# Kernel optimization log

Measured on AMD Instinct MI355X. Metric: run time of the kernel, lower is better.

The kernel has to match this reference:

```python
import jax, jax.numpy as jnp
import numpy as np

H = 4096   # hidden_size
V = 4      # vocab_size (Dyck-2)
OUT = 4    # output_size
MS = 104   # memory_size (stack depth)
MD = 3     # memory_dim (stack element width)


def setup_inputs() -> dict:
    key = jax.random.key(0)
    ks = jax.random.split(key, 17)
    s = 1.0 / np.sqrt(H)
    f32 = jnp.float32
    return {
        "inp": jax.random.randint(ks[0], (1,), 0, H),
        "hidden0": jax.random.normal(ks[1], (1, 1, H), f32),
        "stack": jax.random.normal(ks[2], (MS, MD), f32),
        "emb": (jax.random.normal(ks[3], (H, V), f32) * s),      # nn.Embedding(H, V)
        "w_ih": (jax.random.normal(ks[4], (3 * H, V), f32) * s),  # GRU input weights
        "w_hh": (jax.random.normal(ks[5], (3 * H, H), f32) * s),  # GRU hidden weights
        "b_ih": (jax.random.normal(ks[6], (3 * H,), f32) * s),
        "b_hh": (jax.random.normal(ks[7], (3 * H,), f32) * s),
        "w_y": (jax.random.normal(ks[8], (OUT, H), f32) * s),
        "b_y": (jax.random.normal(ks[9], (OUT,), f32) * s),
        "w_n": (jax.random.normal(ks[10], (MD, H), f32) * s),
        "b_n": (jax.random.normal(ks[11], (MD,), f32) * s),
        "w_a": (jax.random.normal(ks[12], (2, H), f32) * s),
        "b_a": (jax.random.normal(ks[13], (2,), f32) * s),
        "w_sh": (jax.random.normal(ks[14], (H, MD), f32) * s),
        "b_sh": (jax.random.normal(ks[15], (H,), f32) * s),
    }


def reference(inp, hidden0, stack, emb, w_ih, w_hh, b_ih, b_hh,
              w_y, b_y, w_n, b_n, w_a, b_a, w_sh, b_sh):
    # embedded = embedding(inp).view(1,1,-1) -> work with flat (V,)
    x = emb[inp[0]]                                   # (V,)
    # hidden_bar = W_sh(stack[0]) + hidden0
    h_bar = (w_sh @ stack[0] + b_sh) + hidden0[0, 0]  # (H,)
    # one GRU step (PyTorch gate order: r, z, n)
    gi = w_ih @ x + b_ih                              # (3H,)
    gh = w_hh @ h_bar + b_hh                          # (3H,)
    i_r, i_z, i_n = jnp.split(gi, 3)
    h_r, h_z, h_n = jnp.split(gh, 3)
    r = jax.nn.sigmoid(i_r + h_r)
    z = jax.nn.sigmoid(i_z + h_z)
    n = jnp.tanh(i_n + r * h_n)
    h = (1.0 - z) * n + z * h_bar                     # (H,) = ht = hidden
    # heads
    output = jax.nn.sigmoid(w_y @ h + b_y).reshape(1, OUT)
    action = jax.nn.softmax(w_a @ h + b_a)            # (2,) push/pop weights
    new_elt = jax.nn.sigmoid(w_n @ h + b_n).reshape(1, MD)
    # differentiable stack update
    push_side = jnp.concatenate([new_elt, stack[:-1]], axis=0)          # (MS, MD)
    pop_side = jnp.concatenate([stack[1:], jnp.zeros((1, MD), stack.dtype)], axis=0)
    new_stack = action[0] * push_side + action[1] * pop_side
    hidden = h.reshape(1, 1, H)
    return output, hidden, new_stack
```

## Files before the change

### kernel.cpp

```cpp
#include <hip/hip_runtime.h>
#include <hip/hip_bf16.h>

#define H  4096
#define V  4
#define OUT_N 4
#define MS 104
#define MD 3

__device__ __forceinline__ float b2f(unsigned short u) {
    return __uint_as_float(((unsigned int)u) << 16);
}
__device__ __forceinline__ float ldf(const void* p, size_t i, bool is_f32) {
    return is_f32 ? ((const float*)p)[i] : b2f(((const unsigned short*)p)[i]);
}
__device__ __forceinline__ void stf(void* p, size_t i, bool is_f32, float v) {
    if (is_f32) ((float*)p)[i] = v;
    else        ((__hip_bfloat16*)p)[i] = __float2bfloat16(v);
}

__global__ void detect_kernel(const unsigned short* __restrict__ w_hh_raw,
                              int* __restrict__ flag) {
    const int t = threadIdx.x;
    int bad = 0;
    for (int i = t; i < 1024; i += 64) {
        const float v = b2f(w_hh_raw[i]);
        if (!(fabsf(v) < 1.0e6f)) bad = 1;
    }
    const unsigned long long m = __ballot(bad);
    if (t == 0) flag[0] = (m != 0ull) ? 1 : 0;
}

__global__ __launch_bounds__(256) void hbar_kernel(
    const void* __restrict__ w_sh, const void* __restrict__ b_sh,
    const void* __restrict__ hidden0, const void* __restrict__ stack,
    const int* __restrict__ flag, float* __restrict__ h_bar) {
    const bool f32 = flag[0] != 0;
    const float s0 = ldf(stack, 0, f32);
    const float s1 = ldf(stack, 1, f32);
    const float s2 = ldf(stack, 2, f32);
    const int j = blockIdx.x * 256 + threadIdx.x;
    if (j < H) {
        h_bar[j] = ldf(w_sh, (size_t)j * 3 + 0, f32) * s0
                 + ldf(w_sh, (size_t)j * 3 + 1, f32) * s1
                 + ldf(w_sh, (size_t)j * 3 + 2, f32) * s2
                 + ldf(b_sh, j, f32) + ldf(hidden0, j, f32);
    }
}

__global__ __launch_bounds__(256) void gru_kernel(
    const int*  __restrict__ inp,  const void* __restrict__ emb,
    const void* __restrict__ w_ih, const void* __restrict__ w_hh,
    const void* __restrict__ b_ih, const void* __restrict__ b_hh,
    const int*  __restrict__ flag, const float* __restrict__ h_bar,
    float* __restrict__ h_f32, void* __restrict__ out) {
    const bool f32 = flag[0] != 0;
    const int k = blockIdx.x, t = threadIdx.x;
    const size_t r0 = (size_t)k * H;
    const size_t r1 = (size_t)(k + H) * H;
    const size_t r2 = (size_t)(k + 2 * H) * H;

    float ar = 0.f, az = 0.f, an = 0.f;
    #pragma unroll 4
    for (int i = t; i < H; i += 256) {
        const float hb = h_bar[i];
        ar += ldf(w_hh, r0 + i, f32) * hb;
        az += ldf(w_hh, r1 + i, f32) * hb;
        an += ldf(w_hh, r2 + i, f32) * hb;
    }

    #pragma unroll
    for (int off = 32; off > 0; off >>= 1) {
        ar += __shfl_down(ar, off);
        az += __shfl_down(az, off);
        an += __shfl_down(an, off);
    }
    __shared__ float red[4][3];
    const int wave = t >> 6, lane = t & 63;
    if (lane == 0) { red[wave][0] = ar; red[wave][1] = az; red[wave][2] = an; }
    __syncthreads();

    if (t == 0) {
        const float sr = red[0][0] + red[1][0] + red[2][0] + red[3][0];
        const float sz = red[0][1] + red[1][1] + red[2][1] + red[3][1];
        const float sn = red[0][2] + red[1][2] + red[2][2] + red[3][2];

        const int idx = inp[0];
        float x[V];
        #pragma unroll
        for (int c = 0; c < V; ++c) x[c] = ldf(emb, (size_t)idx * V + c, f32);

        float gi[3];
        #pragma unroll
        for (int g = 0; g < 3; ++g) {
            float acc = ldf(b_ih, (size_t)(k + g * H), f32);
            #pragma unroll
            for (int c = 0; c < V; ++c)
                acc += ldf(w_ih, (size_t)(k + g * H) * V + c, f32) * x[c];
            gi[g] = acc;
        }
        const float ghr = sr + ldf(b_hh, (size_t)k,         f32);
        const float ghz = sz + ldf(b_hh, (size_t)(k + H),   f32);
        const float ghn = sn + ldf(b_hh, (size_t)(k + 2*H), f32);

        const float r = 1.f / (1.f + expf(-(gi[0] + ghr)));
        const float z = 1.f / (1.f + expf(-(gi[1] + ghz)));
        const float n = tanhf(gi[2] + r * ghn);
        const float hk = (1.f - z) * n + z * h_bar[k];

        h_f32[k] = hk;
        stf(out, (size_t)(OUT_N + k), f32, hk);
    }
}

__global__ __launch_bounds__(256) void heads_kernel(
    const float* __restrict__ h,
    const void* __restrict__ w_y, const void* __restrict__ b_y,
    const void* __restrict__ w_a, const void* __restrict__ b_a,
    const void* __restrict__ w_n, const void* __restrict__ b_n,
    const void* __restrict__ stack, const int* __restrict__ flag,
    void* __restrict__ out) {
    const bool f32 = flag[0] != 0;
    const int t = threadIdx.x;

    float acc[9];
    #pragma unroll
    for (int s = 0; s < 9; ++s) acc[s] = 0.f;

    for (int i = t; i < H; i += 256) {
        const float hv = h[i];
        #pragma unroll
        for (int s = 0; s < 4; ++s) acc[s]     += ldf(w_y, (size_t)s * H + i, f32) * hv;
        acc[4] += ldf(w_a, (size_t)i,     f32) * hv;
        acc[5] += ldf(w_a, (size_t)H + i, f32) * hv;
        #pragma unroll
        for (int s = 0; s < 3; ++s) acc[6 + s] += ldf(w_n, (size_t)s * H + i, f32) * hv;
    }

    __shared__ float scal[9];
    __shared__ float red[4];
    for (int s = 0; s < 9; ++s) {
        float a = acc[s];
        #pragma unroll
        for (int off = 32; off > 0; off >>= 1) a += __shfl_down(a, off);
        if ((t & 63) == 0) red[t >> 6] = a;
        __syncthreads();
        if (t == 0) scal[s] = red[0] + red[1] + red[2] + red[3];
        __syncthreads();
    }

    __shared__ float act0, act1, ne[MD];
    if (t == 0) {
        const float a0 = scal[4] + ldf(b_a, 0, f32);
        const float a1 = scal[5] + ldf(b_a, 1, f32);
        const float m  = fmaxf(a0, a1);
        const float e0 = expf(a0 - m), e1 = expf(a1 - m);
        const float inv = 1.f / (e0 + e1);
        act0 = e0 * inv; act1 = e1 * inv;
    }
    if (t < OUT_N)
        stf(out, (size_t)t, f32,
            1.f / (1.f + expf(-(scal[t] + ldf(b_y, t, f32)))));
    if (t < MD)
        ne[t] = 1.f / (1.f + expf(-(scal[6 + t] + ldf(b_n, t, f32))));
    __syncthreads();

    const float a0 = act0, a1 = act1;
    for (int idx = t; idx < MS * MD; idx += 256) {
        const int i = idx / MD;
        const int d = idx - i * MD;
        const float push = (i == 0)      ? ne[d] : ldf(stack, (size_t)(idx - MD), f32);
        const float pop  = (i == MS - 1) ? 0.f   : ldf(stack, (size_t)(idx + MD), f32);
        stf(out, (size_t)(OUT_N + H + idx), f32, a0 * push + a1 * pop);
    }
}

extern "C" void kernel_launch(void* const* d_in, const int* in_sizes, int n_in,
                              void* d_out, int out_size, void* d_ws, size_t ws_size,
                              hipStream_t stream) {
    const int* inp      = (const int*)d_in[0];
    const void* hidden0 = d_in[1];
    const void* stack   = d_in[2];
    const void* emb     = d_in[3];
    const void* w_ih    = d_in[4];
    const void* w_hh    = d_in[5];
    const void* b_ih    = d_in[6];
    const void* b_hh    = d_in[7];
    const void* w_y     = d_in[8];
    const void* b_y     = d_in[9];
    const void* w_n     = d_in[10];
    const void* b_n     = d_in[11];
    const void* w_a     = d_in[12];
    const void* b_a     = d_in[13];
    const void* w_sh    = d_in[14];
    const void* b_sh    = d_in[15];

    int*   flag  = (int*)d_ws;
    float* h_bar = (float*)((char*)d_ws + 16);
    float* h     = h_bar + H;

    detect_kernel<<<1, 64, 0, stream>>>((const unsigned short*)w_hh, flag);
    hbar_kernel<<<(H + 255) / 256, 256, 0, stream>>>(w_sh, b_sh, hidden0, stack,
                                                     flag, h_bar);
    gru_kernel<<<H, 256, 0, stream>>>(inp, emb, w_ih, w_hh, b_ih, b_hh,
                                      flag, h_bar, h, d_out);
    heads_kernel<<<1, 256, 0, stream>>>(h, w_y, b_y, w_a, b_a, w_n, b_n,
                                        stack, flag, d_out);
}
```

Measured before the change: 333.3 us.

## Vectorize GRU matvec, map one row per wave, inline dtype detection

Drops the separate dtype-detect kernel and instead has every kernel detect the dtype inline from the first w_hh elements. The GRU matvec now gives each wave one hidden unit and reads w_hh with 128-bit loads (float4 for f32, uint4 holding eight bf16 values). That removes the cross-wave shared-memory reduction and cuts the grid from H blocks to H/4. The heads kernel uses one wave per output row with vectorized loads in a 1024-thread block. The aim is to raise effective bandwidth on the 3H×H weight stream and save one launch, at the cost of redundant detection work in every block.

```diff
diff --git a/kernel.cpp b/kernel.cpp
--- a/kernel.cpp
+++ b/kernel.cpp
@@ -18,54 +18,86 @@
     else        ((__hip_bfloat16*)p)[i] = __float2bfloat16(v);
 }
 
-__global__ void detect_kernel(const unsigned short* __restrict__ w_hh_raw,
-                              int* __restrict__ flag) {
-    const int t = threadIdx.x;
+__device__ __forceinline__ bool detect_f32(const void* w_hh) {
+    const unsigned short* w = (const unsigned short*)w_hh;
+    const int lane = threadIdx.x & 63;
     int bad = 0;
-    for (int i = t; i < 1024; i += 64) {
-        const float v = b2f(w_hh_raw[i]);
+    #pragma unroll
+    for (int i = 0; i < 16; ++i) {
+        const float v = b2f(w[lane + (i << 6)]);
         if (!(fabsf(v) < 1.0e6f)) bad = 1;
     }
-    const unsigned long long m = __ballot(bad);
-    if (t == 0) flag[0] = (m != 0ull) ? 1 : 0;
+    return __ballot(bad) != 0ull;
+}
+
+__device__ __forceinline__ float dot8(uint4 a, float4 h0, float4 h1) {
+    return __uint_as_float(a.x << 16)          * h0.x
+         + __uint_as_float(a.x & 0xffff0000u)  * h0.y
+         + __uint_as_float(a.y << 16)          * h0.z
+         + __uint_as_float(a.y & 0xffff0000u)  * h0.w
+         + __uint_as_float(a.z << 16)          * h1.x
+         + __uint_as_float(a.z & 0xffff0000u)  * h1.y
+         + __uint_as_float(a.w << 16)          * h1.z
+         + __uint_as_float(a.w & 0xffff0000u)  * h1.w;
 }
 
 __global__ __launch_bounds__(256) void hbar_kernel(
     const void* __restrict__ w_sh, const void* __restrict__ b_sh,
     const void* __restrict__ hidden0, const void* __restrict__ stack,
-    const int* __restrict__ flag, float* __restrict__ h_bar) {
-    const bool f32 = flag[0] != 0;
+    const void* __restrict__ w_hh, float* __restrict__ h_bar) {
+    const bool f32 = detect_f32(w_hh);
     const float s0 = ldf(stack, 0, f32);
     const float s1 = ldf(stack, 1, f32);
     const float s2 = ldf(stack, 2, f32);
     const int j = blockIdx.x * 256 + threadIdx.x;
-    if (j < H) {
-        h_bar[j] = ldf(w_sh, (size_t)j * 3 + 0, f32) * s0
-                 + ldf(w_sh, (size_t)j * 3 + 1, f32) * s1
-                 + ldf(w_sh, (size_t)j * 3 + 2, f32) * s2
-                 + ldf(b_sh, j, f32) + ldf(hidden0, j, f32);
-    }
+    h_bar[j] = ldf(w_sh, (size_t)j * 3 + 0, f32) * s0
+             + ldf(w_sh, (size_t)j * 3 + 1, f32) * s1
+             + ldf(w_sh, (size_t)j * 3 + 2, f32) * s2
+             + ldf(b_sh, j, f32) + ldf(hidden0, j, f32);
 }
 
 __global__ __launch_bounds__(256) void gru_kernel(
     const int*  __restrict__ inp,  const void* __restrict__ emb,
     const void* __restrict__ w_ih, const void* __restrict__ w_hh,
     const void* __restrict__ b_ih, const void* __restrict__ b_hh,
-    const int*  __restrict__ flag, const float* __restrict__ h_bar,
-    float* __restrict__ h_f32, void* __restrict__ out) {
-    const bool f32 = flag[0] != 0;
-    const int k = blockIdx.x, t = threadIdx.x;
-    const size_t r0 = (size_t)k * H;
-    const size_t r1 = (size_t)(k + H) * H;
-    const size_t r2 = (size_t)(k + 2 * H) * H;
+    const float* __restrict__ h_bar, float* __restrict__ h_f32,
+    void* __restrict__ out) {
+    const bool f32 = detect_f32(w_hh);
+    const int wave = threadIdx.x >> 6, lane = threadIdx.x & 63;
+    const int k = (blockIdx.x << 2) + wave;
 
     float ar = 0.f, az = 0.f, an = 0.f;
-    #pragma unroll 4
-    for (int i = t; i < H; i += 256) {
-        const float hb = h_bar[i];
-        ar += ldf(w_hh, r0 + i, f32) * hb;
-        az += ldf(w_hh, r1 + i, f32) * hb;
-        an += ldf(w_hh, r2 + i, f32) * hb;
+    if (f32) {
+        const float4* W  = (const float4*)w_hh;
+        const float4* HB = (const float4*)h_bar;
+        const size_t q0 = (size_t)k           * (H / 4);
+        const size_t q1 = (size_t)(k + H)     * (H / 4);
+        const size_t q2 = (size_t)(k + 2 * H) * (H / 4);
+        #pragma unroll 4
+        for (int it = 0; it < H / 256; ++it) {
+            const int i = (it << 6) + lane;
+            const float4 hb = HB[i];
+            const float4 a = W[q0 + i];
+            const float4 b = W[q1 + i];
+            const float4 c = W[q2 + i];
+            ar += a.x * hb.x + a.y * hb.y + a.z * hb.z + a.w * hb.w;
+            az += b.x * hb.x + b.y * hb.y + b.z * hb.z + b.w * hb.w;
+            an += c.x * hb.x + c.y * hb.y + c.z * hb.z + c.w * hb.w;
+        }
+    } else {
+        const uint4*  W  = (const uint4*)w_hh;
+        const float4* HB = (const float4*)h_bar;
+        const size_t q0 = (size_t)k           * (H / 8);
+        const size_t q1 = (size_t)(k + H)     * (H / 8);
+        const size_t q2 = (size_t)(k + 2 * H) * (H / 8);
+        #pragma unroll 2
+        for (int it = 0; it < H / 512; ++it) {
+            const int i = (it << 6) + lane;
+            const float4 h0 = HB[2 * i], h1 = HB[2 * i + 1];
+            ar += dot8(W[q0 + i], h0, h1);
+            az += dot8(W[q1 + i], h0, h1);
+            an += dot8(W[q2 + i], h0, h1);
+        }
     }
 
     #pragma unroll
@@ -74,16 +106,8 @@
         az += __shfl_down(az, off);
         an += __shfl_down(an, off);
     }
-    __shared__ float red[4][3];
-    const int wave = t >> 6, lane = t & 63;
-    if (lane == 0) { red[wave][0] = ar; red[wave][1] = az; red[wave][2] = an; }
-    __syncthreads();
-
-    if (t == 0) {
-        const float sr = red[0][0] + red[1][0] + red[2][0] + red[3][0];
-        const float sz = red[0][1] + red[1][1] + red[2][1] + red[3][1];
-        const float sn = red[0][2] + red[1][2] + red[2][2] + red[3][2];
-
+
+    if (lane == 0) {
         const int idx = inp[0];
         float x[V];
         #pragma unroll
@@ -98,9 +122,9 @@
                 acc += ldf(w_ih, (size_t)(k + g * H) * V + c, f32) * x[c];
             gi[g] = acc;
         }
-        const float ghr = sr + ldf(b_hh, (size_t)k,         f32);
-        const float ghz = sz + ldf(b_hh, (size_t)(k + H),   f32);
-        const float ghn = sn + ldf(b_hh, (size_t)(k + 2*H), f32);
+        const float ghr = ar + ldf(b_hh, (size_t)k,           f32);
+        const float ghz = az + ldf(b_hh, (size_t)(k + H),     f32);
+        const float ghn = an + ldf(b_hh, (size_t)(k + 2 * H), f32);
 
         const float r = 1.f / (1.f + expf(-(gi[0] + ghr)));
         const float z = 1.f / (1.f + expf(-(gi[1] + ghz)));
@@ -112,41 +136,47 @@
     }
 }
 
-__global__ __launch_bounds__(256) void heads_kernel(
+__global__ __launch_bounds__(1024) void heads_kernel(
     const float* __restrict__ h,
     const void* __restrict__ w_y, const void* __restrict__ b_y,
     const void* __restrict__ w_a, const void* __restrict__ b_a,
     const void* __restrict__ w_n, const void* __restrict__ b_n,
-    const void* __restrict__ stack, const int* __restrict__ flag,
+    const void* __restrict__ stack, const void* __restrict__ w_hh,
     void* __restrict__ out) {
-    const bool f32 = flag[0] != 0;
-    const int t = threadIdx.x;
-
-    float acc[9];
-    #pragma unroll
-    for (int s = 0; s < 9; ++s) acc[s] = 0.f;
-
-    for (int i = t; i < H; i += 256) {
-        const float hv = h[i];
+    const bool f32 = detect_f32(w_hh);
+    const int t = threadIdx.x, wave = t >> 6, lane = t & 63;
+
+    __shared__ float scal[9];
+    if (wave < 9) {
+        const void* base; size_t row;
+        if (wave < 4)      { base = w_y; row = (size_t)wave * H; }
+        else if (wave < 6) { base = w_a; row = (size_t)(wave - 4) * H; }
+        else               { base = w_n; row = (size_t)(wave - 6) * H; }
+
+        float acc = 0.f;
+        if (f32) {
+            const float4* W  = (const float4*)((const float*)base + row);
+            const float4* Hv = (const float4*)h;
+            #pragma unroll 4
+            for (int it = 0; it < H / 256; ++it) {
+                const int i = (it << 6) + lane;
+                const float4 a = W[i], hb = Hv[i];
+                acc += a.x * hb.x + a.y * hb.y + a.z * hb.z + a.w * hb.w;
+            }
+        } else {
+            const uint4*  W  = (const uint4*)((const unsigned short*)base + row);
+            const float4* Hv = (const float4*)h;
+            #pragma unroll 2
+            for (int it = 0; it < H / 512; ++it) {
+                const int i = (it << 6) + lane;
+                acc += dot8(W[i], Hv[2 * i], Hv[2 * i + 1]);
+            }
+        }
         #pragma unroll
-        for (int s = 0; s < 4; ++s) acc[s]     += ldf(w_y, (size_t)s * H + i, f32) * hv;
-        acc[4] += ldf(w_a, (size_t)i,     f32) * hv;
-        acc[5] += ldf(w_a, (size_t)H + i, f32) * hv;
-        #pragma unroll
-        for (int s = 0; s < 3; ++s) acc[6 + s] += ldf(w_n, (size_t)s * H + i, f32) * hv;
-    }
-
-    __shared__ float scal[9];
-    __shared__ float red[4];
-    for (int s = 0; s < 9; ++s) {
-        float a = acc[s];
-        #pragma unroll
-        for (int off = 32; off > 0; off >>= 1) a += __shfl_down(a, off);
-        if ((t & 63) == 0) red[t >> 6] = a;
-        __syncthreads();
-        if (t == 0) scal[s] = red[0] + red[1] + red[2] + red[3];
-        __syncthreads();
-    }
+        for (int off = 32; off > 0; off >>= 1) acc += __shfl_down(acc, off);
+        if (lane == 0) scal[wave] = acc;
+    }
+    __syncthreads();
 
     __shared__ float act0, act1, ne[MD];
     if (t == 0) {
@@ -165,7 +195,7 @@
     __syncthreads();
 
     const float a0 = act0, a1 = act1;
-    for (int idx = t; idx < MS * MD; idx += 256) {
+    for (int idx = t; idx < MS * MD; idx += 1024) {
         const int i = idx / MD;
         const int d = idx - i * MD;
         const float push = (i == 0)      ? ne[d] : ldf(stack, (size_t)(idx - MD), f32);
@@ -194,15 +224,13 @@
     const void* w_sh    = d_in[14];
     const void* b_sh    = d_in[15];
 
-    int*   flag  = (int*)d_ws;
-    float* h_bar = (float*)((char*)d_ws + 16);
+    float* h_bar = (float*)d_ws;
     float* h     = h_bar + H;
 
-    detect_kernel<<<1, 64, 0, stream>>>((const unsigned short*)w_hh, flag);
-    hbar_kernel<<<(H + 255) / 256, 256, 0, stream>>>(w_sh, b_sh, hidden0, stack,
-                                                     flag, h_bar);
-    gru_kernel<<<H, 256, 0, stream>>>(inp, emb, w_ih, w_hh, b_ih, b_hh,
-                                      flag, h_bar, h, d_out);
-    heads_kernel<<<1, 256, 0, stream>>>(h, w_y, b_y, w_a, b_a, w_n, b_n,
-                                        stack, flag, d_out);
-}
+    hbar_kernel<<<H / 256, 256, 0, stream>>>(w_sh, b_sh, hidden0, stack,
+                                             w_hh, h_bar);
+    gru_kernel<<<H / 4, 256, 0, stream>>>(inp, emb, w_ih, w_hh, b_ih, b_hh,
+                                          h_bar, h, d_out);
+    heads_kernel<<<1, 1024, 0, stream>>>(h, w_y, b_y, w_a, b_a, w_n, b_n,
+                                         stack, w_hh, d_out);
+}
```

New measurement: 314.1 us. -5.7%, faster.
